# Performance work log

Hardware: AMD Instinct MI355X
Metric: run time of the kernel (lower is better)

The kernel has to match this reference:

```python
import jax, jax.numpy as jnp
import numpy as np

VOCAB = 32000
DEPTH = 18
INNER = VOCAB - 1
EPS = 1e-9


def setup_inputs() -> dict:
    key = jax.random.key(0)
    k_att, k_w, k_idx, k_sign = jax.random.split(key, 4)
    B, T, D = 4, 16, 512
    att = jax.random.normal(k_att, (B, T, D), dtype=jnp.float32)
    # nn.Linear weight, scaled like kaiming-uniform-ish
    W = jax.random.normal(k_w, (INNER, D), dtype=jnp.float32) * (1.0 / np.sqrt(D))
    n = VOCAB * DEPTH
    path_index = jax.random.randint(k_idx, (n,), 0, INNER, dtype=jnp.int32)
    # Huffman path signs: +1 (left child) or -1 (right child)
    path_sign = jnp.where(jax.random.uniform(k_sign, (n,)) < 0.5, 1.0, -1.0).astype(jnp.float32)
    # bias so that prob = sigmoid(h) for left, 1 - sigmoid(h) for right
    path_bias = (1.0 - path_sign) * 0.5
    return {"att": att, "W": W, "path_index": path_index,
            "path_sign": path_sign, "path_bias": path_bias}


def reference(att, W, path_index, path_sign, path_bias):
    B, T, _ = att.shape
    # Linear (no bias) + sigmoid: [B, T, INNER]
    h = jax.nn.sigmoid(jnp.einsum('btd,nd->btn', att, W))
    # gather along inner-node axis to per-(vocab, depth) path probs
    g = jnp.take(h, path_index, axis=-1) * path_sign + path_bias  # [B, T, VOCAB*DEPTH]
    H = g.reshape(B, T, VOCAB, DEPTH)
    H = jnp.clip(H, EPS, 1.0 - EPS)
    logp = jnp.sum(jnp.log(H), axis=-1)  # [B, T, VOCAB]
    return logp
```

## Files before the change

### kernel.cpp

```cpp
#include <hip/hip_runtime.h>
#include <hip/hip_bf16.h>

#define INNER 31999
#define VOCAB 32000
#define DEPTH 18
#define M_DIM 64
#define K_DIM 512
#define LDS_K (K_DIM + 8)

typedef __attribute__((ext_vector_type(8))) short bf16x8;
typedef __attribute__((ext_vector_type(4))) short s16x4;
typedef __attribute__((ext_vector_type(4))) float f32x4;
typedef __attribute__((ext_vector_type(2))) _Float16 f16x2;

__device__ __forceinline__ unsigned int pkbf(float a, float b) {
    const unsigned int ua = __float_as_uint(a) + 0x8000u;
    const unsigned int ub = __float_as_uint(b) + 0x8000u;
    return __builtin_amdgcn_perm(ub, ua, 0x07060302u);
}

__device__ __forceinline__ bf16x8 cvt8(f32x4 lo, f32x4 hi) {
    union { unsigned int u[4]; bf16x8 v; } r;
    r.u[0] = pkbf(lo[0], lo[1]);
    r.u[1] = pkbf(lo[2], lo[3]);
    r.u[2] = pkbf(hi[0], hi[1]);
    r.u[3] = pkbf(hi[2], hi[3]);
    return r.v;
}

__global__ __launch_bounds__(256) void gemm_xt_kernel(
    const float* __restrict__ W,
    const float* __restrict__ att,
    _Float16* __restrict__ xT)
{
    __shared__ __align__(16) unsigned short attb[M_DIM * LDS_K];

    const int tid  = threadIdx.x;
    const int wave = tid >> 6;
    const int lane = tid & 63;
    const int mrow = lane & 15;
    const int quad = lane >> 4;

    #pragma unroll
    for (int i = 0; i < 32; i++) {
        const int f4 = i * 256 + tid;
        const f32x4 v = ((const f32x4*)att)[f4];
        const int f = f4 * 4;
        const int m = f >> 9, k = f & (K_DIM - 1);
        union { unsigned int u[2]; s16x4 s; } o;
        o.u[0] = pkbf(v[0], v[1]);
        o.u[1] = pkbf(v[2], v[3]);
        *(s16x4*)(attb + m * LDS_K + k) = o.s;
    }
    __syncthreads();

    const int n_base = blockIdx.x * 64 + wave * 16;
    const int n = n_base + mrow;
    const int nc = n < INNER ? n : (INNER - 1);
    const float* wp = W + (size_t)nc * K_DIM;

    f32x4 acc[4];
    #pragma unroll
    for (int j = 0; j < 4; j++) acc[j] = (f32x4){0.f, 0.f, 0.f, 0.f};

    #pragma unroll
    for (int k0i = 0; k0i < 16; k0i++) {
        const int koff = k0i * 32 + quad * 8;
        const f32x4* p = (const f32x4*)(wp + koff);
        const bf16x8 a = cvt8(p[0], p[1]);
        #pragma unroll
        for (int j = 0; j < 4; j++) {
            const bf16x8 b = *(const bf16x8*)(attb + (j * 16 + mrow) * LDS_K + koff);
            acc[j] = __builtin_amdgcn_mfma_f32_16x16x32_bf16(a, b, acc[j], 0, 0, 0);
        }
    }

    #pragma unroll
    for (int j = 0; j < 4; j++) {
        const int m = j * 16 + mrow;
        #pragma unroll
        for (int r = 0; r < 4; r++)
            xT[(size_t)(n_base + quad * 4 + r) * M_DIM + m] = (_Float16)acc[j][r];
    }
}

__global__ __launch_bounds__(256) void hsoftmax_kernel(
    const _Float16* __restrict__ xT,
    const int*   __restrict__ path_index,
    const float* __restrict__ path_sign,
    float* __restrict__ out)
{
    __shared__ unsigned int packed[32 * DEPTH];
    __shared__ float2 res2[32][33];

    const int tid = threadIdx.x;
    const int wave = tid >> 6;
    const int lane = tid & 63;
    const int half = lane >> 5;
    const int sub  = lane & 31;
    const int v_base = blockIdx.x * 32;
    const int base = v_base * DEPTH;

    for (int t = tid; t < 32 * DEPTH; t += 256) {
        const unsigned int idx = (unsigned int)path_index[base + t];
        const float s = path_sign[base + t];
        packed[t] = idx | (s < 0.f ? 0x80000000u : 0u);
    }
    __syncthreads();

    for (int i = 0; i < 4; i++) {
        const int vloc = wave * 8 + 2 * i + half;
        float accmin0 = 0.f, accmin1 = 0.f;
        float prod0 = 1.f, prod1 = 1.f;
        #pragma unroll
        for (int d = 0; d < DEPTH; d++) {
            const unsigned int p = packed[vloc * DEPTH + d];
            const unsigned int xx = *(const unsigned int*)(
                (const unsigned short*)xT + (p & 0x7fffu) * M_DIM + sub * 2);
            union { unsigned int u; f16x2 h; } cv; cv.u = xx;
            const float x0 = (float)cv.h[0];
            const float x1 = (float)cv.h[1];
            const unsigned int sgn = p & 0x80000000u;
            const unsigned int xb0 = __float_as_uint(x0);
            const unsigned int xb1 = __float_as_uint(x1);
            const float e0 = __expf(__uint_as_float(xb0 | 0x80000000u));
            const float e1 = __expf(__uint_as_float(xb1 | 0x80000000u));
            prod0 = fmaf(prod0, e0, prod0);
            prod1 = fmaf(prod1, e1, prod1);
            accmin0 += fminf(__uint_as_float(xb0 ^ sgn), 0.f);
            accmin1 += fminf(__uint_as_float(xb1 ^ sgn), 0.f);
        }
        const float r0 = fmaxf(accmin0 - __logf(prod0), -373.1f);
        const float r1 = fmaxf(accmin1 - __logf(prod1), -373.1f);
        res2[vloc][sub] = make_float2(r0, r1);
    }
    __syncthreads();

    #pragma unroll
    for (int it = 0; it < 8; it++) {
        const int m = it * 8 + (tid >> 5);
        const int vloc = tid & 31;
        out[(size_t)m * VOCAB + v_base + vloc] = ((const float*)&res2[vloc][0])[m];
    }
}

extern "C" void kernel_launch(void* const* d_in, const int* in_sizes, int n_in,
                              void* d_out, int out_size, void* d_ws, size_t ws_size,
                              hipStream_t stream) {
    const float* att        = (const float*)d_in[0];
    const float* W          = (const float*)d_in[1];
    const int*   path_index = (const int*)d_in[2];
    const float* path_sign  = (const float*)d_in[3];

    _Float16* xT = (_Float16*)d_ws;
    float* out = (float*)d_out;

    gemm_xt_kernel<<<500, 256, 0, stream>>>(W, att, xT);
    hsoftmax_kernel<<<1000, 256, 0, stream>>>(xT, path_index, path_sign, out);
}
```

Baseline: 121.7 us.

## Pre-convert att to bf16 in MFMA fragment order in a separate kernel

Adds a small kernel that converts att to bf16 once and writes it to workspace in the exact per-lane MFMA B-fragment order. The GEMM blocks then copy that half-size buffer into LDS with straight uint4 loads and read conflict-free, contiguous fragments. This removes the fp32 load and convert work that each of the 500 blocks repeated, at the cost of an extra kernel launch and a workspace round trip.

New measurement: 131.5 us. +8.1%, slower.

```diff
diff --git a/kernel.cpp b/kernel.cpp
--- a/kernel.cpp
+++ b/kernel.cpp
@@ -6,10 +6,8 @@
 #define DEPTH 18
 #define M_DIM 64
 #define K_DIM 512
-#define LDS_K (K_DIM + 8)
 
 typedef __attribute__((ext_vector_type(8))) short bf16x8;
-typedef __attribute__((ext_vector_type(4))) short s16x4;
 typedef __attribute__((ext_vector_type(4))) float f32x4;
 typedef __attribute__((ext_vector_type(2))) _Float16 f16x2;
 
@@ -28,12 +26,31 @@
     return r.v;
 }
 
+__global__ __launch_bounds__(256) void swz_att_kernel(
+    const float* __restrict__ att, unsigned short* __restrict__ attbG)
+{
+    const int t = blockIdx.x * 256 + threadIdx.x;
+    const int lane = t & 63;
+    const int j    = (t >> 6) & 3;
+    const int k0i  = t >> 8;
+    const int mrow = lane & 15;
+    const int quad = lane >> 4;
+    const f32x4* p = (const f32x4*)(att + (j * 16 + mrow) * K_DIM + k0i * 32 + quad * 8);
+    const f32x4 lo = p[0], hi = p[1];
+    uint4 o;
+    o.x = pkbf(lo[0], lo[1]);
+    o.y = pkbf(lo[2], lo[3]);
+    o.z = pkbf(hi[0], hi[1]);
+    o.w = pkbf(hi[2], hi[3]);
+    ((uint4*)attbG)[t] = o;
+}
+
 __global__ __launch_bounds__(256) void gemm_xt_kernel(
     const float* __restrict__ W,
-    const float* __restrict__ att,
+    const unsigned short* __restrict__ attbG,
     _Float16* __restrict__ xT)
 {
-    __shared__ __align__(16) unsigned short attb[M_DIM * LDS_K];
+    __shared__ __align__(16) unsigned short attb[M_DIM * K_DIM];
 
     const int tid  = threadIdx.x;
     const int wave = tid >> 6;
@@ -42,15 +59,9 @@
     const int quad = lane >> 4;
 
     #pragma unroll
-    for (int i = 0; i < 32; i++) {
-        const int f4 = i * 256 + tid;
-        const f32x4 v = ((const f32x4*)att)[f4];
-        const int f = f4 * 4;
-        const int m = f >> 9, k = f & (K_DIM - 1);
-        union { unsigned int u[2]; s16x4 s; } o;
-        o.u[0] = pkbf(v[0], v[1]);
-        o.u[1] = pkbf(v[2], v[3]);
-        *(s16x4*)(attb + m * LDS_K + k) = o.s;
+    for (int i = 0; i < 16; i++) {
+        const int e = i * 256 + tid;
+        ((uint4*)attb)[e] = ((const uint4*)attbG)[e];
     }
     __syncthreads();
 
@@ -70,7 +81,7 @@
         const bf16x8 a = cvt8(p[0], p[1]);
         #pragma unroll
         for (int j = 0; j < 4; j++) {
-            const bf16x8 b = *(const bf16x8*)(attb + (j * 16 + mrow) * LDS_K + koff);
+            const bf16x8 b = *(const bf16x8*)(attb + ((k0i * 4 + j) * 64 + lane) * 8);
             acc[j] = __builtin_amdgcn_mfma_f32_16x16x32_bf16(a, b, acc[j], 0, 0, 0);
         }
     }
@@ -153,8 +164,10 @@
     const float* path_sign  = (const float*)d_in[3];
 
     _Float16* xT = (_Float16*)d_ws;
+    unsigned short* attbG = (unsigned short*)((char*)d_ws + (size_t)VOCAB * M_DIM * 2);
     float* out = (float*)d_out;
 
-    gemm_xt_kernel<<<500, 256, 0, stream>>>(W, att, xT);
+    swz_att_kernel<<<16, 256, 0, stream>>>(att, attbG);
+    gemm_xt_kernel<<<500, 256, 0, stream>>>(W, attbG, xT);
     hsoftmax_kernel<<<1000, 256, 0, stream>>>(xT, path_index, path_sign, out);
 }
```
